# Kernel tuning notes

Hardware: AMD Instinct MI355X
Metric: run time of the kernel (lower is better)

## Reference

```python
import jax, jax.numpy as jnp
import numpy as np

B = 65536      # total rows = env_batch(8192) * n_slave(8)
DIN = 256      # input_shape
H = 64         # slave_hidden_dim
A = 32         # attention_dim
NACT = 14      # n_actions
NS = 8         # n_slave


def setup_inputs() -> dict:
    key = jax.random.key(0)
    ks = jax.random.split(key, 12)
    s = 0.05
    return {
        "obs": jax.random.normal(ks[0], (B, DIN), jnp.float32),
        "hidden_state": jax.random.normal(ks[1], (B, H), jnp.float32),
        "enc_W": jax.random.normal(ks[2], (DIN, H), jnp.float32) * s,
        "enc_b": jnp.zeros((H,), jnp.float32),
        "gru_Wih": jax.random.normal(ks[3], (3 * H, H), jnp.float32) * s,
        "gru_Whh": jax.random.normal(ks[4], (3 * H, H), jnp.float32) * s,
        "gru_bih": jnp.zeros((3 * H,), jnp.float32),
        "gru_bhh": jnp.zeros((3 * H,), jnp.float32),
        "qW": jax.random.normal(ks[5], (H, A), jnp.float32) * s,
        "kW": jax.random.normal(ks[6], (H, A), jnp.float32) * s,
        "vW": jax.random.normal(ks[7], (H, A), jnp.float32) * s,
        "vb": jnp.zeros((A,), jnp.float32),
        "decW": jax.random.normal(ks[8], (H + A, NACT), jnp.float32) * s,
        "decb": jnp.zeros((NACT,), jnp.float32),
        "n_slave": NS,
    }


def reference(obs, hidden_state, enc_W, enc_b, gru_Wih, gru_Whh, gru_bih, gru_bhh,
              qW, kW, vW, vb, decW, decb, n_slave):
    # encoding + ReLU
    x = jax.nn.relu(obs @ enc_W + enc_b)                      # [B, H]
    # torch GRUCell: r,z,n gate order in weight rows
    gx = x @ gru_Wih.T + gru_bih                              # [B, 3H]
    gh = hidden_state @ gru_Whh.T + gru_bhh                   # [B, 3H]
    xr, xz, xn = jnp.split(gx, 3, axis=-1)
    hr, hz, hn = jnp.split(gh, 3, axis=-1)
    r = jax.nn.sigmoid(xr + hr)
    z = jax.nn.sigmoid(xz + hz)
    n = jnp.tanh(xn + r * hn)
    h_out = (1.0 - z) * n + z * hidden_state                  # [B, H]

    Ad = qW.shape[-1]
    q = (h_out @ qW).reshape(-1, n_slave, Ad)                 # [b, n, A]
    k = (h_out @ kW).reshape(-1, n_slave, Ad)
    v = jax.nn.relu(h_out @ vW + vb).reshape(-1, n_slave, Ad)

    # exclude-self attention == diagonal-masked softmax attention
    scores = jnp.einsum('bia,bja->bij', q, k) / jnp.sqrt(jnp.float32(Ad))
    eye = jnp.eye(n_slave, dtype=bool)
    scores = jnp.where(eye, jnp.float32(-1e9), scores)
    attn = jax.nn.softmax(scores, axis=-1)                    # [b, n, n]
    xatt = jnp.einsum('bij,bja->bia', attn, v).reshape(-1, Ad)  # [B, A]

    out = jnp.concatenate([h_out, xatt], axis=-1) @ decW + decb  # [B, n_actions]
    return (out, h_out)
```

## Files before the change

kernel.cpp:

```cpp
#include <hip/hip_runtime.h>


#define NACT 14
#define BTOT 65536

typedef unsigned int  u32;
typedef unsigned short u16;
using short8 = __attribute__((ext_vector_type(8))) short;
using f32x4  = __attribute__((ext_vector_type(4))) float;

#define ENC0 0
#define WIH0 16384
#define WHH0 28672
#define QKV0 40960
#define DEC0 47104
#define WTOT 48640

#define WIHL 0
#define WHHL 12288
#define QKVL 24576
#define DECL 30720
#define DATA0 32256
#define BIASL 69120
#define LDSU16 69632

__device__ __align__(16) u16   g_wbuf[WTOT];
__device__ __align__(16) float g_bias[256];

__device__ __forceinline__ u32 f2bf_rne(float f){
  u32 x = __float_as_uint(f);
  return (x + 0x7fffu + ((x >> 16) & 1u)) >> 16;
}
__device__ __forceinline__ u32 pk2(float a, float b){
  u32 d;
  asm("v_cvt_pk_bf16_f32 %0, %1, %2" : "=v"(d) : "v"(a), "v"(b));
  return d;
}
__device__ __forceinline__ float blo(u32 u){ return __uint_as_float(u << 16); }
__device__ __forceinline__ float bhi(u32 u){ return __uint_as_float(u & 0xffff0000u); }
__device__ __forceinline__ float sigm(float x){ return 1.0f / (1.0f + __expf(-x)); }
__device__ __forceinline__ float tanhp(float x){ return 1.0f - 2.0f / (__expf(2.0f * x) + 1.0f); }
__device__ __forceinline__ short8 as_s8(uint4 v){ union { uint4 u; short8 s; } x; x.u = v; return x.s; }

#define MFMA16(a,b,c) __builtin_amdgcn_mfma_f32_16x16x32_bf16((a),(b),(c),0,0,0)

__global__ void prep(const float* __restrict__ encW, const float* __restrict__ Wih,
                     const float* __restrict__ Whh,  const float* __restrict__ qW,
                     const float* __restrict__ kW,   const float* __restrict__ vW,
                     const float* __restrict__ decW, const float* __restrict__ bih,
                     const float* __restrict__ bhh)
{
  int j = blockIdx.x * 256 + threadIdx.x;
  if (blockIdx.x == 0) {
    int n = threadIdx.x & 63, g = threadIdx.x >> 6;
    float v;
    if      (g == 0) v = bih[n]       + bhh[n];
    else if (g == 1) v = bih[64 + n]  + bhh[64 + n];
    else if (g == 2) v = bih[128 + n];
    else             v = bhh[128 + n];
    g_bias[threadIdx.x] = v;
  }
  if (j >= WTOT) return;
  int pos  = j & 511;
  int lane = pos >> 3, jj = pos & 7;
  int quad = lane >> 4, l16 = lane & 15;
  float val = 0.f;
  if (j < WIH0) {
    int f = j >> 9, ks = f >> 2, t = f & 3;
    int k = ks * 32 + quad * 8 + jj, n = 16 * t + l16;
    val = encW[k * 64 + n];
  } else if (j < WHH0) {
    int f = (j - WIH0) >> 9;
    int u = f / 6, g = (f >> 1) % 3, ks = f & 1;
    int wrow = 64 * g + 16 * u + l16, k = ks * 32 + quad * 8 + jj;
    val = Wih[wrow * 64 + k];
  } else if (j < QKV0) {
    int f = (j - WHH0) >> 9;
    int u = f / 6, g = (f >> 1) % 3, ks = f & 1;
    int wrow = 64 * g + 16 * u + l16, k = ks * 32 + quad * 8 + jj;
    val = Whh[wrow * 64 + k];
  } else if (j < DEC0) {
    int f = (j - QKV0) >> 9, t = f >> 1, ks = f & 1;
    int n = 16 * t + l16, mtx = n >> 5, nn = n & 31;
    int k = ks * 32 + quad * 8 + jj;
    val = (mtx == 0) ? qW[k * 32 + nn] * 0.17677669529663687f
        : (mtx == 1) ? kW[k * 32 + nn] : vW[k * 32 + nn];
  } else {
    int f = (j - DEC0) >> 9;
    int k = f * 32 + quad * 8 + jj, n = l16;
    if (n < 14) val = decW[k * 14 + n];
  }
  g_wbuf[j] = (u16)f2bf_rne(val);
}

template<bool LAST>
__device__ __forceinline__ void tile_body(
    int gr, int grN,
    u16* __restrict__ Xb, const u16* __restrict__ wl, const float* __restrict__ biasL,
    const float* __restrict__ obs, const float* __restrict__ hid,
    const float* __restrict__ encb, const float* __restrict__ vb,
    const float* __restrict__ decb, float* __restrict__ out,
    float4 (&pre)[2][2], float4 (&preN)[2][2],
    int lane, int quad, int l16)
{
  u16*   Hb = Xb + 1152;
  float* Sf = (float*)(Xb + 2304);

  float4 hv[4];
  #pragma unroll
  for (int i = 0; i < 4; i++) {
    int c = lane + 64 * i;
    hv[i] = ((const float4*)hid)[(size_t)(gr + (c >> 4)) * 16 + (c & 15)];
  }
  #pragma unroll
  for (int i = 0; i < 4; i++) {
    int c = lane + 64 * i;
    int lr = c >> 4, c4 = c & 15;
    *(uint2*)&Hb[lr * 72 + c4 * 4] = make_uint2(pk2(hv[i].x, hv[i].y), pk2(hv[i].z, hv[i].w));
  }

  f32x4 ce[4];
  #pragma unroll
  for (int t = 0; t < 4; t++) {
    float bv = encb[16 * t + l16];
    ce[t] = (f32x4){bv, bv, bv, bv};
  }
  #pragma unroll
  for (int ks = 0; ks < 8; ks++) {
    const int s = ks & 1;
    float4 a0 = pre[s][0], a1 = pre[s][1];
    short8 a = as_s8(make_uint4(pk2(a0.x, a0.y), pk2(a0.z, a0.w), pk2(a1.x, a1.y), pk2(a1.z, a1.w)));
    if (ks < 6) {
      const float* ap = obs + (size_t)(gr + l16) * 256 + (ks + 2) * 32 + quad * 8;
      pre[s][0] = *(const float4*)ap;
      pre[s][1] = *(const float4*)(ap + 4);
    }
    #pragma unroll
    for (int t = 0; t < 4; t++) {
      short8 b = as_s8(*(const uint4*)&g_wbuf[ENC0 + (ks * 4 + t) * 512 + lane * 8]);
      ce[t] = MFMA16(a, b, ce[t]);
    }
  }
  if (!LAST) {
    const float* ap = obs + (size_t)(grN + l16) * 256 + quad * 8;
    preN[0][0] = *(const float4*)ap;        preN[0][1] = *(const float4*)(ap + 4);
    preN[1][0] = *(const float4*)(ap + 32); preN[1][1] = *(const float4*)(ap + 36);
  }
  #pragma unroll
  for (int t = 0; t < 4; t++)
    #pragma unroll
    for (int r = 0; r < 4; r++) {
      float xv = fmaxf(ce[t][r], 0.f);
      Xb[(quad * 4 + r) * 72 + 16 * t + l16] = (u16)pk2(xv, xv);
    }

  short8 ax[2], ah[2];
  #pragma unroll
  for (int ks = 0; ks < 2; ks++) {
    ax[ks] = *(const short8*)&Xb[l16 * 72 + ks * 32 + quad * 8];
    ah[ks] = *(const short8*)&Hb[l16 * 72 + ks * 32 + quad * 8];
  }
  #pragma unroll
  for (int u = 0; u < 4; u++) {
    f32x4 g6[6];
    #pragma unroll
    for (int t = 0; t < 6; t++) g6[t] = (f32x4){0.f, 0.f, 0.f, 0.f};
    #pragma unroll
    for (int g = 0; g < 3; g++) {
      #pragma unroll
      for (int ks = 0; ks < 2; ks++) {
        int f = (u * 3 + g) * 2 + ks;
        short8 bi = *(const short8*)&wl[WIHL + f * 512 + lane * 8];
        short8 bh = *(const short8*)&wl[WHHL + f * 512 + lane * 8];
        g6[g]     = MFMA16(ax[ks], bi, g6[g]);
        g6[3 + g] = MFMA16(ah[ks], bh, g6[3 + g]);
      }
    }
    int nc = 16 * u + l16;
    float brz = biasL[nc], bzz = biasL[64 + nc], bni = biasL[128 + nc], bnh = biasL[192 + nc];
    float hp[4];
    #pragma unroll
    for (int r = 0; r < 4; r++)
      hp[r] = blo(Hb[(quad * 4 + r) * 72 + nc]);
    #pragma unroll
    for (int r = 0; r < 4; r++) {
      float rg = sigm(g6[0][r] + g6[3][r] + brz);
      float zg = sigm(g6[1][r] + g6[4][r] + bzz);
      float nn = tanhp(g6[2][r] + bni + rg * (g6[5][r] + bnh));
      float ho = (1.f - zg) * nn + zg * hp[r];
      Hb[(quad * 4 + r) * 72 + nc] = (u16)pk2(ho, ho);
    }
  }

  short8 hx[2];
  #pragma unroll
  for (int ks = 0; ks < 2; ks++)
    hx[ks] = *(const short8*)&Hb[l16 * 72 + ks * 32 + quad * 8];
  f32x4 cq[6];
  #pragma unroll
  for (int t = 0; t < 6; t++) {
    float bv = (t >= 4) ? vb[16 * (t - 4) + l16] : 0.f;
    cq[t] = (f32x4){bv, bv, bv, bv};
  }
  #pragma unroll
  for (int ks = 0; ks < 2; ks++)
    #pragma unroll
    for (int t = 0; t < 6; t++) {
      short8 b = *(const short8*)&wl[QKVL + (t * 2 + ks) * 512 + lane * 8];
      cq[t] = MFMA16(hx[ks], b, cq[t]);
    }
  #pragma unroll
  for (int t = 0; t < 4; t++)
    #pragma unroll
    for (int r = 0; r < 4; r++)
      Sf[(quad * 4 + r) * 68 + 16 * t + l16] = cq[t][r];
  #pragma unroll
  for (int t = 4; t < 6; t++)
    #pragma unroll
    for (int r = 0; r < 4; r++)
      Xb[(quad * 4 + r) * 72 + 32 + 16 * (t - 4) + l16] =
          (u16)pk2(fmaxf(cq[t][r], 0.f), 0.f);

  {
    const int r_l = lane >> 2, s4 = lane & 3;
    const int gb = r_l & ~7, ri = r_l & 7;
    const float* fq = &Sf[r_l * 68];
    float sc[2];
    #pragma unroll
    for (int jj = 0; jj < 2; jj++) {
      int j = 2 * s4 + jj;
      const float* fk = &Sf[(gb + j) * 68 + 32];
      float d = 0.f;
      #pragma unroll
      for (int a4 = 0; a4 < 32; a4 += 4) {
        float4 q4 = *(const float4*)&fq[a4];
        float4 k4 = *(const float4*)&fk[a4];
        d += q4.x * k4.x + q4.y * k4.y + q4.z * k4.z + q4.w * k4.w;
      }
      sc[jj] = (j == ri) ? -1e30f : d;
    }
    float m = fmaxf(sc[0], sc[1]);
    m = fmaxf(m, __shfl_xor(m, 1));
    m = fmaxf(m, __shfl_xor(m, 2));
    float p[2], sum = 0.f;
    #pragma unroll
    for (int jj = 0; jj < 2; jj++) {
      int j = 2 * s4 + jj;
      p[jj] = (j == ri) ? 0.f : __expf(sc[jj] - m);
      sum += p[jj];
    }
    sum += __shfl_xor(sum, 1);
    sum += __shfl_xor(sum, 2);
    float inv = 1.f / sum;
    #pragma unroll
    for (int jj = 0; jj < 2; jj++)
      Sf[r_l * 68 + 2 * s4 + jj] = p[jj] * inv;
    float xa[8];
    #pragma unroll
    for (int u = 0; u < 8; u++) xa[u] = 0.f;
    #pragma unroll
    for (int j = 0; j < 8; j++) {
      float aj = Sf[r_l * 68 + j];
      const u16* vp = &Xb[(gb + j) * 72 + 32 + 8 * s4];
      uint4 v0 = *(const uint4*)vp;
      xa[0] += aj * blo(v0.x); xa[1] += aj * bhi(v0.x);
      xa[2] += aj * blo(v0.y); xa[3] += aj * bhi(v0.y);
      xa[4] += aj * blo(v0.z); xa[5] += aj * bhi(v0.z);
      xa[6] += aj * blo(v0.w); xa[7] += aj * bhi(v0.w);
    }
    u16* xp = &Xb[r_l * 72 + 8 * s4];
    *(uint4*)xp = make_uint4(pk2(xa[0], xa[1]), pk2(xa[2], xa[3]),
                             pk2(xa[4], xa[5]), pk2(xa[6], xa[7]));
  }

  {
    float db = (l16 < NACT) ? decb[l16] : 0.f;
    f32x4 co = (f32x4){db, db, db, db};
    #pragma unroll
    for (int ks = 0; ks < 2; ks++) {
      short8 b = *(const short8*)&wl[DECL + ks * 512 + lane * 8];
      short8 a = *(const short8*)&Hb[l16 * 72 + ks * 32 + quad * 8];
      co = MFMA16(a, b, co);
    }
    short8 b2 = *(const short8*)&wl[DECL + 2 * 512 + lane * 8];
    short8 a2 = *(const short8*)&Xb[l16 * 72 + quad * 8];
    co = MFMA16(a2, b2, co);
    if (l16 < NACT)
      #pragma unroll
      for (int r = 0; r < 4; r++)
        out[(size_t)(gr + quad * 4 + r) * NACT + l16] = co[r];
  }

  {
    float* outH = out + (size_t)BTOT * NACT;
    #pragma unroll
    for (int i = 0; i < 2; i++) {
      int c = lane + 64 * i, lr = c >> 3, j = c & 7;
      uint4 u = *(const uint4*)&Hb[lr * 72 + 8 * j];
      *(float4*)(outH + (size_t)(gr + lr) * 64 + 8 * j) =
          make_float4(blo(u.x), bhi(u.x), blo(u.y), bhi(u.y));
      *(float4*)(outH + (size_t)(gr + lr) * 64 + 8 * j + 4) =
          make_float4(blo(u.z), bhi(u.z), blo(u.w), bhi(u.w));
    }
  }
}

__global__ __launch_bounds__(512, 2)
void commslave_main(const float* __restrict__ obs,  const float* __restrict__ hid,
                    const float* __restrict__ encb, const float* __restrict__ vb,
                    const float* __restrict__ decb, float* __restrict__ out)
{
  __shared__ __align__(16) u16 lds[LDSU16];

  const int tid  = threadIdx.x;
  const int w    = tid >> 6;
  const int lane = tid & 63;
  const int quad = lane >> 4;
  const int l16  = lane & 15;

  {
    uint4* dw = (uint4*)lds;
    const uint4* sw = (const uint4*)(g_wbuf + WIH0);
    #pragma unroll
    for (int i = 0; i < 8; i++) {
      int idx = tid + 512 * i;
      if (idx < 4032) dw[idx] = sw[idx];
    }
    if (tid < 64) ((uint4*)(lds + BIASL))[tid] = ((const uint4*)g_bias)[tid];
  }

  const int gr0 = blockIdx.x * 256 + w * 16;
  const int gr1 = gr0 + 128;

  float4 pre0[2][2], pre1[2][2];
  {
    const float* ap = obs + (size_t)(gr0 + l16) * 256 + quad * 8;
    pre0[0][0] = *(const float4*)ap;        pre0[0][1] = *(const float4*)(ap + 4);
    pre0[1][0] = *(const float4*)(ap + 32); pre0[1][1] = *(const float4*)(ap + 36);
  }
  __syncthreads();

  u16* Xb = lds + DATA0 + w * 4608;
  const float* biasL = (const float*)(lds + BIASL);

  tile_body<false>(gr0, gr1, Xb, lds, biasL, obs, hid, encb, vb, decb, out,
                   pre0, pre1, lane, quad, l16);
  tile_body<true >(gr1, 0,   Xb, lds, biasL, obs, hid, encb, vb, decb, out,
                   pre1, pre0, lane, quad, l16);
}

extern "C" void kernel_launch(void* const* d_in, const int* in_sizes, int n_in,
                              void* d_out, int out_size, void* d_ws, size_t ws_size,
                              hipStream_t stream) {
  (void)in_sizes; (void)n_in; (void)d_ws; (void)ws_size; (void)out_size;
  const float* obs  = (const float*)d_in[0];
  const float* hid  = (const float*)d_in[1];
  const float* encW = (const float*)d_in[2];
  const float* encb = (const float*)d_in[3];
  const float* Wih  = (const float*)d_in[4];
  const float* Whh  = (const float*)d_in[5];
  const float* bih  = (const float*)d_in[6];
  const float* bhh  = (const float*)d_in[7];
  const float* qW   = (const float*)d_in[8];
  const float* kW   = (const float*)d_in[9];
  const float* vW   = (const float*)d_in[10];
  const float* vb   = (const float*)d_in[11];
  const float* decW = (const float*)d_in[12];
  const float* decb = (const float*)d_in[13];
  float* out = (float*)d_out;

  prep<<<(WTOT + 255) / 256, 256, 0, stream>>>(encW, Wih, Whh, qW, kW, vW, decW, bih, bhh);
  commslave_main<<<256, 512, 0, stream>>>(obs, hid, encb, vb, decb, out);
}
```

Baseline: 147.5 us.

## Prefetch entire obs and hidden tile into registers before compute

Replaces the two-stage rolling obs prefetch with a whole-tile register prefetch (16 float4 of obs plus 4 float4 of hidden per lane). The first tile's loads are issued before the weight copy into LDS, and the second tile's are issued right after the first tile's encoder MFMAs. The goal is more memory-level parallelism and better hiding of global-load latency behind compute. In exchange it uses about 80 more VGPRs per lane, which under launch_bounds(512,2) risks spills or register pressure.

```diff
diff --git a/kernel.cpp b/kernel.cpp
--- a/kernel.cpp
+++ b/kernel.cpp
@@ -93,6 +93,28 @@
   g_wbuf[j] = (u16)f2bf_rne(val);
 }
 
+struct Chunk {
+  float4 ob[16];
+  float4 hv[4];
+};
+
+__device__ __forceinline__ void issue_loads(int gr, const float* __restrict__ obs,
+                                            const float* __restrict__ hid,
+                                            int lane, int quad, int l16, Chunk& c)
+{
+  const float* ap = obs + (size_t)(gr + l16) * 256 + quad * 8;
+  #pragma unroll
+  for (int ks = 0; ks < 8; ks++) {
+    c.ob[2 * ks]     = *(const float4*)(ap + ks * 32);
+    c.ob[2 * ks + 1] = *(const float4*)(ap + ks * 32 + 4);
+  }
+  #pragma unroll
+  for (int i = 0; i < 4; i++) {
+    int cc = lane + 64 * i;
+    c.hv[i] = ((const float4*)hid)[(size_t)(gr + (cc >> 4)) * 16 + (cc & 15)];
+  }
+}
+
 template<bool LAST>
 __device__ __forceinline__ void tile_body(
     int gr, int grN,
@@ -100,23 +122,18 @@
     const float* __restrict__ obs, const float* __restrict__ hid,
     const float* __restrict__ encb, const float* __restrict__ vb,
     const float* __restrict__ decb, float* __restrict__ out,
-    float4 (&pre)[2][2], float4 (&preN)[2][2],
+    Chunk& cur, Chunk& nxt,
     int lane, int quad, int l16)
 {
   u16*   Hb = Xb + 1152;
   float* Sf = (float*)(Xb + 2304);
 
-  float4 hv[4];
-  #pragma unroll
-  for (int i = 0; i < 4; i++) {
-    int c = lane + 64 * i;
-    hv[i] = ((const float4*)hid)[(size_t)(gr + (c >> 4)) * 16 + (c & 15)];
-  }
   #pragma unroll
   for (int i = 0; i < 4; i++) {
     int c = lane + 64 * i;
     int lr = c >> 4, c4 = c & 15;
-    *(uint2*)&Hb[lr * 72 + c4 * 4] = make_uint2(pk2(hv[i].x, hv[i].y), pk2(hv[i].z, hv[i].w));
+    *(uint2*)&Hb[lr * 72 + c4 * 4] =
+        make_uint2(pk2(cur.hv[i].x, cur.hv[i].y), pk2(cur.hv[i].z, cur.hv[i].w));
   }
 
   f32x4 ce[4];
@@ -127,25 +144,15 @@
   }
   #pragma unroll
   for (int ks = 0; ks < 8; ks++) {
-    const int s = ks & 1;
-    float4 a0 = pre[s][0], a1 = pre[s][1];
+    float4 a0 = cur.ob[2 * ks], a1 = cur.ob[2 * ks + 1];
     short8 a = as_s8(make_uint4(pk2(a0.x, a0.y), pk2(a0.z, a0.w), pk2(a1.x, a1.y), pk2(a1.z, a1.w)));
-    if (ks < 6) {
-      const float* ap = obs + (size_t)(gr + l16) * 256 + (ks + 2) * 32 + quad * 8;
-      pre[s][0] = *(const float4*)ap;
-      pre[s][1] = *(const float4*)(ap + 4);
-    }
     #pragma unroll
     for (int t = 0; t < 4; t++) {
       short8 b = as_s8(*(const uint4*)&g_wbuf[ENC0 + (ks * 4 + t) * 512 + lane * 8]);
       ce[t] = MFMA16(a, b, ce[t]);
     }
   }
-  if (!LAST) {
-    const float* ap = obs + (size_t)(grN + l16) * 256 + quad * 8;
-    preN[0][0] = *(const float4*)ap;        preN[0][1] = *(const float4*)(ap + 4);
-    preN[1][0] = *(const float4*)(ap + 32); preN[1][1] = *(const float4*)(ap + 36);
-  }
+  if (!LAST) issue_loads(grN, obs, hid, lane, quad, l16, nxt);
   #pragma unroll
   for (int t = 0; t < 4; t++)
     #pragma unroll
@@ -318,6 +325,12 @@
   const int quad = lane >> 4;
   const int l16  = lane & 15;
 
+  const int gr0 = blockIdx.x * 256 + w * 16;
+  const int gr1 = gr0 + 128;
+
+  Chunk c0, c1;
+  issue_loads(gr0, obs, hid, lane, quad, l16, c0);
+
   {
     uint4* dw = (uint4*)lds;
     const uint4* sw = (const uint4*)(g_wbuf + WIH0);
@@ -328,25 +341,15 @@
     }
     if (tid < 64) ((uint4*)(lds + BIASL))[tid] = ((const uint4*)g_bias)[tid];
   }
-
-  const int gr0 = blockIdx.x * 256 + w * 16;
-  const int gr1 = gr0 + 128;
-
-  float4 pre0[2][2], pre1[2][2];
-  {
-    const float* ap = obs + (size_t)(gr0 + l16) * 256 + quad * 8;
-    pre0[0][0] = *(const float4*)ap;        pre0[0][1] = *(const float4*)(ap + 4);
-    pre0[1][0] = *(const float4*)(ap + 32); pre0[1][1] = *(const float4*)(ap + 36);
-  }
   __syncthreads();
 
   u16* Xb = lds + DATA0 + w * 4608;
   const float* biasL = (const float*)(lds + BIASL);
 
   tile_body<false>(gr0, gr1, Xb, lds, biasL, obs, hid, encb, vb, decb, out,
-                   pre0, pre1, lane, quad, l16);
+                   c0, c1, lane, quad, l16);
   tile_body<true >(gr1, 0,   Xb, lds, biasL, obs, hid, encb, vb, decb, out,
-                   pre1, pre0, lane, quad, l16);
+                   c1, c0, lane, quad, l16);
 }
 
 extern "C" void kernel_launch(void* const* d_in, const int* in_sizes, int n_in,
```

Result: no change. 144.8 us (-1.8%).
